# Kernel optimization log

Hardware: AMD Instinct MI355X
Metric: run time of the kernel (lower is better)

## Reference

```python
import jax, jax.numpy as jnp
import numpy as np

N_PARTS = 24


def setup_inputs() -> dict:
    key = jax.random.key(0)
    k1, k2, k3, k4 = jax.random.split(key, 4)
    B, C, R = 8, 16, 512
    H = W = 512
    tex = jax.random.normal(k1, (B, C, R, R), dtype=jnp.float32)
    # iuv: channel 0 = part id in [0, 24] (0 == background), channels 1,2 = UV bytes in [0, 255]
    part = jax.random.randint(k2, (B, 1, H, W), 0, N_PARTS + 1, dtype=jnp.int32)
    uv = jax.random.randint(k3, (B, 2, H, W), 0, 256, dtype=jnp.int32)
    iuv = jnp.concatenate([part, uv], axis=1)
    lut = jax.random.uniform(k4, (N_PARTS, 256, 256, 2), dtype=jnp.float32)
    return {"tex": tex, "iuv": iuv, "lut": lut, "tex_res": R}


def reference(tex, iuv, lut, tex_res):
    # tex: [B, C, R, R], iuv: [B, 3, H, W] int, lut: [24, 256, 256, 2]
    B = tex.shape[0]
    mask = iuv[:, 0] > 0                                   # [B, H, W]
    i = jnp.clip(iuv[:, 0] - 1, 0, lut.shape[0] - 1)       # part index, clamped for masked-out pixels
    u = jnp.clip(iuv[:, 1].astype(jnp.float32) / 255.0, 0.0, 1.0)
    v = jnp.clip(iuv[:, 2].astype(jnp.float32) / 255.0, 0.0, 1.0)
    ui = jnp.round(u * 255.0).astype(jnp.int32)
    vi = jnp.round(v * 255.0).astype(jnp.int32)
    uv_smpl = lut[i, vi, ui]                               # [B, H, W, 2]
    u_I = jnp.round(uv_smpl[..., 0] * (tex_res - 1)).astype(jnp.int32)
    v_I = jnp.round((1.0 - uv_smpl[..., 1]) * (tex_res - 1)).astype(jnp.int32)
    b_idx = jnp.arange(B)[:, None, None]                   # [B, 1, 1]
    gathered = tex[b_idx, :, v_I, u_I]                     # [B, H, W, C]
    out = jnp.where(mask[..., None], gathered, jnp.zeros((), tex.dtype))
    return jnp.transpose(out, (0, 3, 1, 2))                # [B, C, H, W]
```

## Files before the change

### kernel.cpp

```cpp
#include <hip/hip_runtime.h>


#define N_PARTS 24

typedef float v4f __attribute__((ext_vector_type(4)));
typedef int   v4i __attribute__((ext_vector_type(4)));

__global__ __launch_bounds__(256) void dp_transpose_kernel(
    const float* __restrict__ tex,
    float*       __restrict__ texT)
{
    constexpr int C = 16, R = 512;
    constexpr size_t plane = (size_t)R * R;
    __shared__ float lds[16 * 516];

    const int tid = blockIdx.x;
    const int b  = tid >> 9;
    const int ty = tid & 511;
    const float* src = tex + (size_t)b * C * plane + (size_t)ty * R;
    const int t = threadIdx.x;

    #pragma unroll
    for (int k = 0; k < 8; ++k) {
        const int f  = k * 256 + t;
        const int c  = f >> 7;
        const int x4 = f & 127;
        const v4f v = __builtin_nontemporal_load(
            (const v4f*)(src + (size_t)c * plane + x4 * 4));
        *(v4f*)&lds[c * 516 + x4 * 4] = v;
    }
    __syncthreads();
    float* dst = texT + ((size_t)b * plane + (size_t)ty * R) * C;
    #pragma unroll
    for (int k = 0; k < 8; ++k) {
        const int f  = k * 256 + t;
        const int x  = f >> 2;
        const int c0 = (f & 3) * 4;
        v4f v;
        v.x = lds[(c0 + 0) * 516 + x];
        v.y = lds[(c0 + 1) * 516 + x];
        v.z = lds[(c0 + 2) * 516 + x];
        v.w = lds[(c0 + 3) * 516 + x];
        __builtin_nontemporal_store(v, (v4f*)(dst + (size_t)f * 4));
    }
}

__global__ __launch_bounds__(256) void dp_offsets_kernel(
    const int*   __restrict__ iuv,
    const float* __restrict__ lut,
    int*         __restrict__ offs,
    int R)
{
    constexpr int H = 512, W = 512;
    const float scale = (float)(R - 1);
    const size_t hw = (size_t)H * W;
    const int t = blockIdx.x * blockDim.x + threadIdx.x;
    const int pix4 = t * 4;
    const int b = pix4 >> 18;
    const int p = pix4 & (int)(hw - 1);

    const size_t ibase = (size_t)b * 3 * hw + p;
    const v4i p4 = __builtin_nontemporal_load((const v4i*)(iuv + ibase));
    const v4i u4 = __builtin_nontemporal_load((const v4i*)(iuv + ibase + hw));
    const v4i v4 = __builtin_nontemporal_load((const v4i*)(iuv + ibase + 2 * hw));

    const int parts[4] = {p4.x, p4.y, p4.z, p4.w};
    const int us[4]    = {u4.x, u4.y, u4.z, u4.w};
    const int vs[4]    = {v4.x, v4.y, v4.z, v4.w};

    v4i o4;
    #pragma unroll
    for (int j = 0; j < 4; ++j) {
        int i = parts[j] - 1;
        i = i < 0 ? 0 : (i > N_PARTS - 1 ? N_PARTS - 1 : i);
        const float fu = fminf(fmaxf((float)us[j] / 255.0f, 0.0f), 1.0f);
        const float fv = fminf(fmaxf((float)vs[j] / 255.0f, 0.0f), 1.0f);
        const int ui = (int)rintf(fu * 255.0f);
        const int vi = (int)rintf(fv * 255.0f);
        const float2 s = *(const float2*)(lut + (((size_t)i * 256 + vi) * 256 + ui) * 2);
        const int uI = (int)rintf(s.x * scale);
        const int vI = (int)rintf((1.0f - s.y) * scale);
        const int o = (parts[j] > 0) ? (vI * R + uI) : -1;
        if (j == 0) o4.x = o; else if (j == 1) o4.y = o;
        else if (j == 2) o4.z = o; else o4.w = o;
    }
    __builtin_nontemporal_store(o4, (v4i*)(offs + (size_t)b * hw + p));
}

__global__ __launch_bounds__(256) void dp_gatherT_kernel(
    const float* __restrict__ texT,
    const int*   __restrict__ offs,
    float*       __restrict__ out)
{
    constexpr int C = 16;
    constexpr size_t HW = 512 * 512;
    __shared__ float lds[16 * 256];
    extern __shared__ float occupancy_pad[];

    const int b     = blockIdx.x & 7;
    const int inner = blockIdx.x >> 3;
    const int base  = inner * 1024;

    const float* tb   = texT + (size_t)b * HW * C;
    const int*   ob   = offs + (size_t)b * HW + base;
    float*       outb = out  + (size_t)b * C * HW + base;
    const int t = threadIdx.x;

    for (int tile = 0; tile < 4; ++tile) {
        const int p = tile * 256 + t;
        const int o = __builtin_nontemporal_load(ob + p);
        const bool m = o >= 0;
        const v4f* src = (const v4f*)(tb + (size_t)(m ? o : 0) * C);
        v4f r0 = src[0];
        v4f r1 = src[1];
        v4f r2 = src[2];
        v4f r3 = src[3];
        if (!m) {
            r0 = 0.f; r1 = 0.f; r2 = 0.f; r3 = 0.f;
        }

        if (tile) __syncthreads();
        lds[ 0 * 256 + t] = r0.x;  lds[ 1 * 256 + t] = r0.y;
        lds[ 2 * 256 + t] = r0.z;  lds[ 3 * 256 + t] = r0.w;
        lds[ 4 * 256 + t] = r1.x;  lds[ 5 * 256 + t] = r1.y;
        lds[ 6 * 256 + t] = r1.z;  lds[ 7 * 256 + t] = r1.w;
        lds[ 8 * 256 + t] = r2.x;  lds[ 9 * 256 + t] = r2.y;
        lds[10 * 256 + t] = r2.z;  lds[11 * 256 + t] = r2.w;
        lds[12 * 256 + t] = r3.x;  lds[13 * 256 + t] = r3.y;
        lds[14 * 256 + t] = r3.z;  lds[15 * 256 + t] = r3.w;
        __syncthreads();

        #pragma unroll
        for (int k = 0; k < 4; ++k) {
            const int idx = k * 256 + t;
            const int c   = idx >> 6;
            const int p4  = idx & 63;
            const v4f v = *(const v4f*)&lds[c * 256 + p4 * 4];
            __builtin_nontemporal_store(
                v, (v4f*)(outb + (size_t)c * HW + tile * 256 + p4 * 4));
        }
    }
}

__global__ __launch_bounds__(256) void dp_gather_kernel(
    const float* __restrict__ tex,
    const int*   __restrict__ offs,
    float*       __restrict__ out,
    int R)
{
    constexpr int C = 16, H = 512, W = 512;
    const size_t hw    = (size_t)H * W;
    const size_t plane = (size_t)R * R;

    const int bid  = blockIdx.x;
    const int xcd  = bid & 7;
    const int slot = bid >> 3;
    const int pl_local = slot >> 8;
    const int inner    = slot & 255;
    const int pidx = xcd * 16 + pl_local;
    const int b = pidx >> 4;
    const int c = pidx & 15;

    const int px = inner * 1024 + threadIdx.x * 4;

    const int4 o4 = *(const int4*)(offs + (size_t)b * hw + px);
    const float* tc = tex + ((size_t)b * C + c) * plane;

    float4 r;
    r.x = (o4.x >= 0) ? tc[o4.x] : 0.0f;
    r.y = (o4.y >= 0) ? tc[o4.y] : 0.0f;
    r.z = (o4.z >= 0) ? tc[o4.z] : 0.0f;
    r.w = (o4.w >= 0) ? tc[o4.w] : 0.0f;

    *(float4*)(out + ((size_t)b * C + c) * hw + px) = r;
}

extern "C" void kernel_launch(void* const* d_in, const int* in_sizes, int n_in,
                              void* d_out, int out_size, void* d_ws, size_t ws_size,
                              hipStream_t stream) {
    const float* tex = (const float*)d_in[0];
    const int*   iuv = (const int*)d_in[1];
    const float* lut = (const float*)d_in[2];
    float*       out = (float*)d_out;

    constexpr int B = 8, C = 16, H = 512, W = 512;
    int R = 512;
    {
        long long pe = (long long)in_sizes[0] / (B * C);
        int r = 1; while ((long long)(r + 1) * (r + 1) <= pe) ++r;
        R = r;
    }

    const size_t texT_bytes = (size_t)B * R * R * C * sizeof(float);
    const size_t offs_bytes = (size_t)B * H * W * sizeof(int);

    if (R == 512 && ws_size >= texT_bytes + offs_bytes) {
        float* texT = (float*)d_ws;
        int*   offs = (int*)((char*)d_ws + texT_bytes);
        dp_transpose_kernel<<<dim3(4096), dim3(256), 0, stream>>>(tex, texT);
        dp_offsets_kernel<<<dim3(B * H * W / 4 / 256), dim3(256), 0, stream>>>(
            iuv, lut, offs, R);
        dp_gatherT_kernel<<<dim3(2048), dim3(256), 45056, stream>>>(
            texT, offs, out);
    } else if (ws_size >= offs_bytes) {
        int* offs = (int*)d_ws;
        dp_offsets_kernel<<<dim3(B * H * W / 4 / 256), dim3(256), 0, stream>>>(
            iuv, lut, offs, R);
        dp_gather_kernel<<<dim3(B * C * (H * W / 1024)), dim3(256), 0, stream>>>(
            tex, offs, out, R);
    }
}
```

Baseline: 346.2 us.

## Make gather transpose wave-local and prefetch next pixel's texels

The gather kernel now gives each wavefront its own LDS slice and its own 256 pixels. This removes the block-wide __syncthreads between tiles. It also loads all four offsets up front and double-buffers the 64-byte texel gathers, so the next gather is in flight while the current one is written through LDS. In exchange, each channel's output store now covers 256 contiguous bytes instead of 1 KB, and correctness relies on LDS ordering inside a wavefront with no explicit wave barrier.

```diff
diff --git a/kernel.cpp b/kernel.cpp
--- a/kernel.cpp
+++ b/kernel.cpp
@@ -94,51 +94,62 @@
 {
     constexpr int C = 16;
     constexpr size_t HW = 512 * 512;
-    __shared__ float lds[16 * 256];
+    __shared__ float lds[4 * 1024];
     extern __shared__ float occupancy_pad[];
 
     const int b     = blockIdx.x & 7;
     const int inner = blockIdx.x >> 3;
     const int base  = inner * 1024;
 
+    const int t    = threadIdx.x;
+    const int lane = t & 63;
+    const int wv   = t >> 6;
+
     const float* tb   = texT + (size_t)b * HW * C;
-    const int*   ob   = offs + (size_t)b * HW + base;
-    float*       outb = out  + (size_t)b * C * HW + base;
-    const int t = threadIdx.x;
-
-    for (int tile = 0; tile < 4; ++tile) {
-        const int p = tile * 256 + t;
-        const int o = __builtin_nontemporal_load(ob + p);
-        const bool m = o >= 0;
-        const v4f* src = (const v4f*)(tb + (size_t)(m ? o : 0) * C);
-        v4f r0 = src[0];
-        v4f r1 = src[1];
-        v4f r2 = src[2];
-        v4f r3 = src[3];
-        if (!m) {
-            r0 = 0.f; r1 = 0.f; r2 = 0.f; r3 = 0.f;
+    const int*   obw  = offs + (size_t)b * HW + base + wv * 256;
+    float*       outb = out  + (size_t)b * C * HW + base + wv * 256;
+    float*       wlds = lds + wv * 1024;
+
+    int o[4];
+    #pragma unroll
+    for (int i = 0; i < 4; ++i)
+        o[i] = __builtin_nontemporal_load(obw + i * 64 + lane);
+
+    v4f c0, c1, c2, c3;
+    {
+        const v4f* src = (const v4f*)(tb + (size_t)(o[0] >= 0 ? o[0] : 0) * C);
+        c0 = src[0]; c1 = src[1]; c2 = src[2]; c3 = src[3];
+    }
+
+    #pragma unroll
+    for (int iter = 0; iter < 4; ++iter) {
+        v4f n0 = 0.f, n1 = 0.f, n2 = 0.f, n3 = 0.f;
+        if (iter < 3) {
+            const int on = o[iter + 1];
+            const v4f* src = (const v4f*)(tb + (size_t)(on >= 0 ? on : 0) * C);
+            n0 = src[0]; n1 = src[1]; n2 = src[2]; n3 = src[3];
         }
 
-        if (tile) __syncthreads();
-        lds[ 0 * 256 + t] = r0.x;  lds[ 1 * 256 + t] = r0.y;
-        lds[ 2 * 256 + t] = r0.z;  lds[ 3 * 256 + t] = r0.w;
-        lds[ 4 * 256 + t] = r1.x;  lds[ 5 * 256 + t] = r1.y;
-        lds[ 6 * 256 + t] = r1.z;  lds[ 7 * 256 + t] = r1.w;
-        lds[ 8 * 256 + t] = r2.x;  lds[ 9 * 256 + t] = r2.y;
-        lds[10 * 256 + t] = r2.z;  lds[11 * 256 + t] = r2.w;
-        lds[12 * 256 + t] = r3.x;  lds[13 * 256 + t] = r3.y;
-        lds[14 * 256 + t] = r3.z;  lds[15 * 256 + t] = r3.w;
-        __syncthreads();
+        if (o[iter] < 0) { c0 = 0.f; c1 = 0.f; c2 = 0.f; c3 = 0.f; }
+        wlds[ 0 * 64 + lane] = c0.x;  wlds[ 1 * 64 + lane] = c0.y;
+        wlds[ 2 * 64 + lane] = c0.z;  wlds[ 3 * 64 + lane] = c0.w;
+        wlds[ 4 * 64 + lane] = c1.x;  wlds[ 5 * 64 + lane] = c1.y;
+        wlds[ 6 * 64 + lane] = c1.z;  wlds[ 7 * 64 + lane] = c1.w;
+        wlds[ 8 * 64 + lane] = c2.x;  wlds[ 9 * 64 + lane] = c2.y;
+        wlds[10 * 64 + lane] = c2.z;  wlds[11 * 64 + lane] = c2.w;
+        wlds[12 * 64 + lane] = c3.x;  wlds[13 * 64 + lane] = c3.y;
+        wlds[14 * 64 + lane] = c3.z;  wlds[15 * 64 + lane] = c3.w;
 
         #pragma unroll
         for (int k = 0; k < 4; ++k) {
-            const int idx = k * 256 + t;
-            const int c   = idx >> 6;
-            const int p4  = idx & 63;
-            const v4f v = *(const v4f*)&lds[c * 256 + p4 * 4];
+            const v4f v = *(const v4f*)&wlds[k * 256 + lane * 4];
+            const int c = k * 4 + (lane >> 4);
+            const int s = lane & 15;
             __builtin_nontemporal_store(
-                v, (v4f*)(outb + (size_t)c * HW + tile * 256 + p4 * 4));
+                v, (v4f*)(outb + (size_t)c * HW + iter * 64 + s * 4));
         }
+
+        c0 = n0; c1 = n1; c2 = n2; c3 = n3;
     }
 }
 
```

Result: faster. 338.8 us (-2.1%).
